# Performance work log

Hardware: AMD Instinct MI355X
Metric: run time of the kernel (lower is better)

Reference implementation:

```python
import jax, jax.numpy as jnp
import numpy as np

B, S, D = 2, 2048, 1024
H = 8
HD = D // H  # 128
RANK = 4
CONTROL_SCALE = 1.0


def setup_inputs() -> dict:
    key = jax.random.key(0)
    ks = jax.random.split(key, 8)
    sd = 0.02
    return {
        "hidden_states": jax.random.normal(ks[0], (B, S, D), jnp.float32),
        "control_states": jax.random.normal(ks[1], (B, S, D), jnp.float32),
        "Wq": jax.random.normal(ks[2], (D, D), jnp.float32) * sd,
        "Wk": jax.random.normal(ks[3], (D, D), jnp.float32) * sd,
        "Wv": jax.random.normal(ks[4], (D, D), jnp.float32) * sd,
        "Wo": jax.random.normal(ks[5], (D, D), jnp.float32) * sd,
        "bo": jnp.zeros((D,), jnp.float32),
        "lora_down": jax.random.normal(ks[6], (RANK, D), jnp.float32) * sd,
        "lora_up": jax.random.normal(ks[7], (D, RANK), jnp.float32) * sd,
    }


def _split_heads(x):  # [B,S,D] -> [B,H,S,HD]
    return x.reshape(B, S, H, HD).transpose(0, 2, 1, 3)


def reference(hidden_states, control_states, Wq, Wk, Wv, Wo, bo, lora_down, lora_up):
    # q/k/v projections (Linear, no bias); self-attention (encoder_hidden_states=None)
    q = _split_heads(jnp.einsum("bsd,ed->bse", hidden_states, Wq))
    k = _split_heads(jnp.einsum("bsd,ed->bse", hidden_states, Wk))
    v = _split_heads(jnp.einsum("bsd,ed->bse", hidden_states, Wv))
    inv_sqrt_d = 1.0 / jnp.sqrt(jnp.asarray(HD, q.dtype))
    scores = jnp.einsum("bhqd,bhkd->bhqk", q, k) * inv_sqrt_d  # [B,H,S,S]
    probs = jax.nn.softmax(scores, axis=-1)
    attn_out = jnp.einsum("bhqk,bhkd->bhqd", probs, v)  # [B,H,S,HD]
    attn_out = attn_out.transpose(0, 2, 1, 3).reshape(B, S, D)
    # to_out[0] Linear with bias; to_out[1] Dropout is identity at eval
    out = jnp.einsum("bsd,ed->bse", attn_out, Wo) + bo
    # LoRA control injection: up(down(control_states))
    ctrl = jnp.einsum("bsr,er->bse", jnp.einsum("bsd,rd->bsr", control_states, lora_down), lora_up)
    return out + CONTROL_SCALE * ctrl
```

## Files before the change

kernel.cpp:

```cpp
#include <hip/hip_runtime.h>
#include <hip/hip_bf16.h>


typedef __bf16 bf8_t __attribute__((ext_vector_type(8)));
typedef float f32x4 __attribute__((ext_vector_type(4)));
typedef float f32x16 __attribute__((ext_vector_type(16)));
typedef unsigned u32x4 __attribute__((ext_vector_type(4)));

#define MFMA16(a, b, c) __builtin_amdgcn_mfma_f32_16x16x32_bf16((a), (b), (c), 0, 0, 0)
#define MFMA32(a, b, c) __builtin_amdgcn_mfma_f32_32x32x16_bf16((a), (b), (c), 0, 0, 0)

__device__ __forceinline__ void gload_lds16(const void* g, void* l) {
  __builtin_amdgcn_global_load_lds(
      (const __attribute__((address_space(1))) void*)g,
      (__attribute__((address_space(3))) void*)l, 16, 0, 0);
}

__device__ __forceinline__ unsigned pk2(float a, float b) {
  unsigned short ua = __builtin_bit_cast(unsigned short, (__bf16)a);
  unsigned short ub = __builtin_bit_cast(unsigned short, (__bf16)b);
  return (unsigned)ua | ((unsigned)ub << 16);
}

__global__ __launch_bounds__(256) void cvt5_k(
    const float* __restrict__ s0, const float* __restrict__ s1,
    const float* __restrict__ s2, const float* __restrict__ s3,
    const float* __restrict__ s4, __bf16* __restrict__ d0,
    __bf16* __restrict__ d1, __bf16* __restrict__ d2, __bf16* __restrict__ d3,
    __bf16* __restrict__ d4) {
  const int which = blockIdx.y;
  const float* s = (which == 0) ? s0 : (which == 1) ? s1 : (which == 2) ? s2
                   : (which == 3) ? s3 : s4;
  __bf16* d = (which == 0) ? d0 : (which == 1) ? d1 : (which == 2) ? d2
              : (which == 3) ? d3 : d4;
  const int n = (which == 0) ? (4096 * 1024) : (1024 * 1024);
  const int i = (blockIdx.x * 256 + threadIdx.x) * 8;
  if (i >= n) return;
  float4 a = *(const float4*)(s + i);
  float4 b = *(const float4*)(s + i + 4);
  bf8_t r;
  r[0] = (__bf16)a.x; r[1] = (__bf16)a.y; r[2] = (__bf16)a.z; r[3] = (__bf16)a.w;
  r[4] = (__bf16)b.x; r[5] = (__bf16)b.y; r[6] = (__bf16)b.z; r[7] = (__bf16)b.w;
  *(bf8_t*)(d + i) = r;
}

__device__ __forceinline__ void gemm_tile(const __bf16* __restrict__ Abase,
                                          const __bf16* __restrict__ Wbase,
                                          int K, __bf16* sA, __bf16* sB,
                                          f32x4 acc[4][4]) {
  const int tid = threadIdx.x;
  const int wave = tid >> 6, lane = tid & 63;
  const int wr = (wave >> 1) * 64, wc = (wave & 1) * 64;
  const int lrow = lane >> 3, lchunk = lane & 7;

  for (int m = 0; m < 4; ++m)
    for (int n = 0; n < 4; ++n)
      acc[m][n] = f32x4{0.f, 0.f, 0.f, 0.f};

  for (int k0 = 0; k0 < K; k0 += 64) {
    for (int i = 0; i < 4; ++i) {
      const int rbase = i * 32 + wave * 8;
      gload_lds16(Abase + (size_t)(rbase + lrow) * K + k0 + lchunk * 8,
                  sA + rbase * 64);
      gload_lds16(Wbase + (size_t)(rbase + lrow) * K + k0 + lchunk * 8,
                  sB + rbase * 64);
    }
    __syncthreads();

    for (int kk = 0; kk < 2; ++kk) {
      bf8_t af[4], bfr[4];
      const int koff = kk * 32 + (lane >> 4) * 8;
      for (int m = 0; m < 4; ++m)
        af[m] = *(const bf8_t*)&sA[(wr + m * 16 + (lane & 15)) * 64 + koff];
      for (int n = 0; n < 4; ++n)
        bfr[n] = *(const bf8_t*)&sB[(wc + n * 16 + (lane & 15)) * 64 + koff];
      for (int m = 0; m < 4; ++m)
        for (int n = 0; n < 4; ++n)
          acc[m][n] = MFMA16(af[m], bfr[n], acc[m][n]);
    }
    __syncthreads();
  }
}

__global__ __launch_bounds__(256) void gemm_qkv_k(
    const __bf16* __restrict__ X, const __bf16* __restrict__ Wq,
    const __bf16* __restrict__ Wk, const __bf16* __restrict__ Wv,
    __bf16* __restrict__ Qb, __bf16* __restrict__ Kb, __bf16* __restrict__ Vtb) {
  __shared__ __bf16 sA[128 * 64];
  __shared__ __bf16 sB[128 * 64];
  const int z = blockIdx.z;
  const int K = 1024;
  int rowT, colT, Nout;
  const __bf16 *Abase, *Wbase;
  __bf16* C;
  if (z == 2) {
    rowT = blockIdx.x; colT = blockIdx.y; Nout = 4096;
    Abase = Wv + (size_t)rowT * 128 * K;
    Wbase = X + (size_t)colT * 128 * K;
    C = Vtb;
  } else {
    rowT = blockIdx.y; colT = blockIdx.x; Nout = 1024;
    Abase = X + (size_t)rowT * 128 * K;
    Wbase = ((z == 0) ? Wq : Wk) + (size_t)colT * 128 * K;
    C = (z == 0) ? Qb : Kb;
  }
  f32x4 acc[4][4];
  gemm_tile(Abase, Wbase, K, sA, sB, acc);

  const int lane = threadIdx.x & 63, wave = threadIdx.x >> 6;
  const int wr = (wave >> 1) * 64, wc = (wave & 1) * 64;
  const int row0 = rowT * 128 + wr + (lane >> 4) * 4;
  const int col0 = colT * 128 + wc + (lane & 15);
  for (int m = 0; m < 4; ++m)
    for (int n = 0; n < 4; ++n)
      for (int j = 0; j < 4; ++j)
        C[(size_t)(row0 + m * 16 + j) * Nout + col0 + n * 16] = (__bf16)acc[m][n][j];
}

__global__ __launch_bounds__(256) void lora_down_k(
    const float* __restrict__ ctrl, const float* __restrict__ down,
    float* __restrict__ tmp) {
  const int tid = threadIdx.x, wave = tid >> 6, lane = tid & 63;
  const int s = blockIdx.x * 4 + wave;
  const float* cp = ctrl + (size_t)s * 1024 + lane * 16;
  float4 c[4];
  for (int i = 0; i < 4; ++i) c[i] = *(const float4*)(cp + i * 4);
  for (int r = 0; r < 4; ++r) {
    const float* dp = down + r * 1024 + lane * 16;
    float acc = 0.f;
    for (int i = 0; i < 4; ++i) {
      float4 dv = *(const float4*)(dp + i * 4);
      acc += c[i].x * dv.x + c[i].y * dv.y + c[i].z * dv.z + c[i].w * dv.w;
    }
    for (int off = 32; off > 0; off >>= 1) acc += __shfl_xor(acc, off);
    if (lane == 0) tmp[s * 4 + r] = acc;
  }
}

__global__ __launch_bounds__(128) void flash_attn_k(
    const __bf16* __restrict__ Qg, const __bf16* __restrict__ Kg,
    const __bf16* __restrict__ Vtg, __bf16* __restrict__ Og) {
  const int S = 2048, D = 1024;
  __shared__ __bf16 sK[2][64 * 128];
  __shared__ __bf16 sVt[2][128 * 64];
  __shared__ float sW[2][32];
  const int qt = blockIdx.x, bh = blockIdx.y;
  const int b = bh >> 3, h = bh & 7;
  const int tid = threadIdx.x, wave = tid >> 6, lane = tid & 63;
  const int l31 = lane & 31, hi = lane >> 5;
  const size_t base = (size_t)b * S * D + (size_t)h * 128;
  const size_t vtbase = (size_t)h * 128 * 4096 + (size_t)b * 2048;
  const int q0 = qt * 64 + wave * 32;

  bf8_t qf[8];
  {
    const float c = 0.08838834764831845f * 1.4426950408889634f;
    const __bf16* qp = Qg + base + (size_t)(q0 + l31) * D + hi * 8;
#pragma unroll
    for (int dc = 0; dc < 8; ++dc) {
      bf8_t v = *(const bf8_t*)(qp + dc * 16);
#pragma unroll
      for (int j = 0; j < 8; ++j) v[j] = (__bf16)((float)v[j] * c);
      qf[dc] = v;
    }
  }

  f32x16 accO[4];
#pragma unroll
  for (int db = 0; db < 4; ++db)
#pragma unroll
    for (int j = 0; j < 16; ++j) accO[db][j] = 0.f;
  float m_ = -1e30f, l_ = 0.f;

  auto stageK = [&](int buf, int kv) {
#pragma unroll
    for (int i = 0; i < 8; ++i) {
      const int r = wave * 32 + i * 4 + (lane >> 4);
      const int gc = (lane & 15) ^ (r & 7);
      gload_lds16(Kg + base + (size_t)(kv + r) * D + gc * 8,
                  &sK[buf][(wave * 32 + i * 4) * 128]);
    }
  };
  auto stageV = [&](int buf, int kv) {
#pragma unroll
    for (int i = 0; i < 8; ++i) {
      const int d = wave * 64 + i * 8 + (lane >> 3);
      const int gc = (lane & 7) ^ (d & 7);
      gload_lds16(Vtg + vtbase + (size_t)d * 4096 + kv + gc * 8,
                  &sVt[buf][(wave * 64 + i * 8) * 64]);
    }
  };

  stageK(0, 0);
  stageV(0, 0);

  for (int t = 0; t < 32; ++t) {
    const int cur = t & 1;
    __syncthreads();
    if (t < 31) {
      stageK(cur ^ 1, (t + 1) * 64);
      stageV(cur ^ 1, (t + 1) * 64);
    }

    f32x16 accS[2];
#pragma unroll
    for (int kb = 0; kb < 2; ++kb)
#pragma unroll
      for (int j = 0; j < 16; ++j) accS[kb][j] = 0.f;
    const __bf16* kb_ = sK[cur];
#pragma unroll
    for (int kb = 0; kb < 2; ++kb) {
      const int kr = kb * 32 + l31;
#pragma unroll
      for (int dc = 0; dc < 8; ++dc) {
        bf8_t a = *(const bf8_t*)&kb_[kr * 128 + ((2 * dc + hi) ^ (kr & 7)) * 8];
        accS[kb] = MFMA32(a, qf[dc], accS[kb]);
      }
    }

    float pm = accS[0][0];
#pragma unroll
    for (int j = 1; j < 16; ++j) pm = fmaxf(pm, accS[0][j]);
#pragma unroll
    for (int j = 0; j < 16; ++j) pm = fmaxf(pm, accS[1][j]);
    pm = fmaxf(pm, __shfl_xor(pm, 32));

    if (__ballot(pm > m_ + 8.0f)) {
      const float mn = fmaxf(m_, pm);
      const float sc = exp2f(m_ - mn);
      m_ = mn;
      l_ *= sc;
      if (hi == 0) sW[wave][l31] = sc;
#pragma unroll
      for (int r = 0; r < 16; ++r) {
        const float scr = sW[wave][(r & 3) + 8 * (r >> 2) + 4 * hi];
#pragma unroll
        for (int db = 0; db < 4; ++db) accO[db][r] *= scr;
      }
    }

    float rs = 0.f;
#pragma unroll
    for (int kb = 0; kb < 2; ++kb)
#pragma unroll
      for (int j = 0; j < 16; ++j) {
        const float p = exp2f(accS[kb][j] - m_);
        accS[kb][j] = p;
        rs += p;
      }
    rs += __shfl_xor(rs, 32);
    l_ += rs;

    unsigned pk[2][4][2];
#pragma unroll
    for (int kb = 0; kb < 2; ++kb)
#pragma unroll
      for (int tq = 0; tq < 4; ++tq) {
        pk[kb][tq][0] = pk2(accS[kb][4 * tq + 0], accS[kb][4 * tq + 1]);
        pk[kb][tq][1] = pk2(accS[kb][4 * tq + 2], accS[kb][4 * tq + 3]);
      }

    const __bf16* vt_ = sVt[cur];
#pragma unroll
    for (int kc = 0; kc < 4; ++kc) {
      const int kb = kc >> 1, par = kc & 1;
      const unsigned own0 = hi ? pk[kb][2 * par + 1][0] : pk[kb][2 * par][0];
      const unsigned own1 = hi ? pk[kb][2 * par + 1][1] : pk[kb][2 * par][1];
      const unsigned snd0 = hi ? pk[kb][2 * par][0] : pk[kb][2 * par + 1][0];
      const unsigned snd1 = hi ? pk[kb][2 * par][1] : pk[kb][2 * par + 1][1];
      const unsigned rc0 = (unsigned)__shfl_xor((int)snd0, 32);
      const unsigned rc1 = (unsigned)__shfl_xor((int)snd1, 32);
      u32x4 fr;
      fr[0] = hi ? rc0 : own0;
      fr[1] = hi ? rc1 : own1;
      fr[2] = hi ? own0 : rc0;
      fr[3] = hi ? own1 : rc1;
      const bf8_t pa = __builtin_bit_cast(bf8_t, fr);
#pragma unroll
      for (int db = 0; db < 4; ++db) {
        const int dr = db * 32 + l31;
        bf8_t vb = *(const bf8_t*)&vt_[dr * 64 + ((2 * kc + hi) ^ (dr & 7)) * 8];
        accO[db] = MFMA32(pa, vb, accO[db]);
      }
    }
  }

  if (hi == 0) sW[wave][l31] = l_;
#pragma unroll
  for (int r = 0; r < 16; ++r) {
    const int qr = (r & 3) + 8 * (r >> 2) + 4 * hi;
    const float linv = 1.0f / sW[wave][qr];
    __bf16* op = Og + base + (size_t)(q0 + qr) * D + l31;
#pragma unroll
    for (int db = 0; db < 4; ++db)
      op[db * 32] = (__bf16)(accO[db][r] * linv);
  }
}

__global__ __launch_bounds__(256) void gemm_out_k(
    const __bf16* __restrict__ A, const __bf16* __restrict__ Wo,
    const float* __restrict__ bo, const float* __restrict__ lup,
    const float* __restrict__ tmp, float* __restrict__ out) {
  __shared__ __bf16 sA[128 * 64];
  __shared__ __bf16 sB[128 * 64];
  const int bcol = blockIdx.x, brow = blockIdx.y;
  const int K = 1024, N = 1024;
  f32x4 acc[4][4];
  gemm_tile(A + (size_t)brow * 128 * K, Wo + (size_t)bcol * 128 * K, K, sA, sB, acc);

  const int lane = threadIdx.x & 63, wave = threadIdx.x >> 6;
  const int wr = (wave >> 1) * 64, wc = (wave & 1) * 64;
  for (int n = 0; n < 4; ++n) {
    const int col = bcol * 128 + wc + n * 16 + (lane & 15);
    const float bias = bo[col];
    const float u0 = lup[col * 4 + 0], u1 = lup[col * 4 + 1];
    const float u2 = lup[col * 4 + 2], u3 = lup[col * 4 + 3];
    for (int m = 0; m < 4; ++m)
      for (int j = 0; j < 4; ++j) {
        const int row = brow * 128 + wr + m * 16 + (lane >> 4) * 4 + j;
        const float* t = tmp + row * 4;
        float v = acc[m][n][j] + bias + t[0] * u0 + t[1] * u1 + t[2] * u2 + t[3] * u3;
        out[(size_t)row * N + col] = v;
      }
  }
}

extern "C" void kernel_launch(void* const* d_in, const int* in_sizes, int n_in,
                              void* d_out, int out_size, void* d_ws, size_t ws_size,
                              hipStream_t stream) {
  (void)in_sizes; (void)n_in; (void)out_size; (void)ws_size;
  const float* hs  = (const float*)d_in[0];
  const float* cs  = (const float*)d_in[1];
  const float* Wq  = (const float*)d_in[2];
  const float* Wk  = (const float*)d_in[3];
  const float* Wv  = (const float*)d_in[4];
  const float* Wo  = (const float*)d_in[5];
  const float* bo  = (const float*)d_in[6];
  const float* ldw = (const float*)d_in[7];
  const float* lup = (const float*)d_in[8];
  float* out = (float*)d_out;

  const size_t MD = (size_t)4096 * 1024;
  const size_t WD = (size_t)1024 * 1024;
  __bf16* hsb = (__bf16*)d_ws;
  __bf16* Wqb = hsb + MD;
  __bf16* Wkb = Wqb + WD;
  __bf16* Wvb = Wkb + WD;
  __bf16* Wob = Wvb + WD;
  __bf16* Qb  = Wob + WD;
  __bf16* Kb  = Qb + MD;
  __bf16* Vtb = Kb + MD;
  __bf16* Ab  = Vtb + MD;
  float*  tmp = (float*)(Ab + MD);

  cvt5_k<<<dim3(2048, 5), 256, 0, stream>>>(hs, Wq, Wk, Wv, Wo,
                                            hsb, Wqb, Wkb, Wvb, Wob);
  gemm_qkv_k<<<dim3(8, 32, 3), 256, 0, stream>>>(hsb, Wqb, Wkb, Wvb, Qb, Kb, Vtb);
  lora_down_k<<<dim3(1024), 256, 0, stream>>>(cs, ldw, tmp);
  flash_attn_k<<<dim3(32, 16), 128, 0, stream>>>(Qb, Kb, Vtb, Ab);
  gemm_out_k<<<dim3(8, 32), 256, 0, stream>>>(Ab, Wob, bo, lup, tmp, out);
}
```

Before: 176.0 us.

## Split attention KV range across two blocks and merge partial results

```diff
diff --git a/kernel.cpp b/kernel.cpp
--- a/kernel.cpp
+++ b/kernel.cpp
@@ -139,18 +139,20 @@
 
 __global__ __launch_bounds__(128) void flash_attn_k(
     const __bf16* __restrict__ Qg, const __bf16* __restrict__ Kg,
-    const __bf16* __restrict__ Vtg, __bf16* __restrict__ Og) {
+    const __bf16* __restrict__ Vtg, __bf16* __restrict__ Op,
+    float* __restrict__ ml) {
   const int S = 2048, D = 1024;
-  __shared__ __bf16 sK[2][64 * 128];
-  __shared__ __bf16 sVt[2][128 * 64];
+  __shared__ __bf16 sK[2][32 * 128];
+  __shared__ __bf16 sVt[2][128 * 32];
   __shared__ float sW[2][32];
-  const int qt = blockIdx.x, bh = blockIdx.y;
+  const int qt = blockIdx.x, bh = blockIdx.y, z = blockIdx.z;
   const int b = bh >> 3, h = bh & 7;
   const int tid = threadIdx.x, wave = tid >> 6, lane = tid & 63;
   const int l31 = lane & 31, hi = lane >> 5;
   const size_t base = (size_t)b * S * D + (size_t)h * 128;
   const size_t vtbase = (size_t)h * 128 * 4096 + (size_t)b * 2048;
   const int q0 = qt * 64 + wave * 32;
+  const int kvbase = z * 1024;
 
   bf8_t qf[8];
   {
@@ -174,55 +176,48 @@
 
   auto stageK = [&](int buf, int kv) {
 #pragma unroll
-    for (int i = 0; i < 8; ++i) {
-      const int r = wave * 32 + i * 4 + (lane >> 4);
+    for (int i = 0; i < 4; ++i) {
+      const int r = wave * 16 + i * 4 + (lane >> 4);
       const int gc = (lane & 15) ^ (r & 7);
       gload_lds16(Kg + base + (size_t)(kv + r) * D + gc * 8,
-                  &sK[buf][(wave * 32 + i * 4) * 128]);
+                  &sK[buf][(wave * 16 + i * 4) * 128]);
     }
   };
   auto stageV = [&](int buf, int kv) {
 #pragma unroll
-    for (int i = 0; i < 8; ++i) {
-      const int d = wave * 64 + i * 8 + (lane >> 3);
-      const int gc = (lane & 7) ^ (d & 7);
+    for (int i = 0; i < 4; ++i) {
+      const int d = wave * 64 + i * 16 + (lane >> 2);
+      const int gc = (lane & 3) ^ (d & 3);
       gload_lds16(Vtg + vtbase + (size_t)d * 4096 + kv + gc * 8,
-                  &sVt[buf][(wave * 64 + i * 8) * 64]);
+                  &sVt[buf][(wave * 64 + i * 16) * 32]);
     }
   };
 
-  stageK(0, 0);
-  stageV(0, 0);
+  stageK(0, kvbase);
+  stageV(0, kvbase);
 
   for (int t = 0; t < 32; ++t) {
     const int cur = t & 1;
     __syncthreads();
     if (t < 31) {
-      stageK(cur ^ 1, (t + 1) * 64);
-      stageV(cur ^ 1, (t + 1) * 64);
-    }
-
-    f32x16 accS[2];
-#pragma unroll
-    for (int kb = 0; kb < 2; ++kb)
-#pragma unroll
-      for (int j = 0; j < 16; ++j) accS[kb][j] = 0.f;
+      stageK(cur ^ 1, kvbase + (t + 1) * 32);
+      stageV(cur ^ 1, kvbase + (t + 1) * 32);
+    }
+
+    f32x16 accS;
+#pragma unroll
+    for (int j = 0; j < 16; ++j) accS[j] = 0.f;
     const __bf16* kb_ = sK[cur];
-#pragma unroll
-    for (int kb = 0; kb < 2; ++kb) {
-      const int kr = kb * 32 + l31;
-#pragma unroll
-      for (int dc = 0; dc < 8; ++dc) {
-        bf8_t a = *(const bf8_t*)&kb_[kr * 128 + ((2 * dc + hi) ^ (kr & 7)) * 8];
-        accS[kb] = MFMA32(a, qf[dc], accS[kb]);
-      }
-    }
-
-    float pm = accS[0][0];
-#pragma unroll
-    for (int j = 1; j < 16; ++j) pm = fmaxf(pm, accS[0][j]);
-#pragma unroll
-    for (int j = 0; j < 16; ++j) pm = fmaxf(pm, accS[1][j]);
+    const int kr = l31;
+#pragma unroll
+    for (int dc = 0; dc < 8; ++dc) {
+      bf8_t a = *(const bf8_t*)&kb_[kr * 128 + ((2 * dc + hi) ^ (kr & 7)) * 8];
+      accS = MFMA32(a, qf[dc], accS);
+    }
+
+    float pm = accS[0];
+#pragma unroll
+    for (int j = 1; j < 16; ++j) pm = fmaxf(pm, accS[j]);
     pm = fmaxf(pm, __shfl_xor(pm, 32));
 
     if (__ballot(pm > m_ + 8.0f)) {
@@ -241,33 +236,28 @@
 
     float rs = 0.f;
 #pragma unroll
-    for (int kb = 0; kb < 2; ++kb)
-#pragma unroll
-      for (int j = 0; j < 16; ++j) {
-        const float p = exp2f(accS[kb][j] - m_);
-        accS[kb][j] = p;
-        rs += p;
-      }
+    for (int j = 0; j < 16; ++j) {
+      const float p = exp2f(accS[j] - m_);
+      accS[j] = p;
+      rs += p;
+    }
     rs += __shfl_xor(rs, 32);
     l_ += rs;
 
-    unsigned pk[2][4][2];
-#pragma unroll
-    for (int kb = 0; kb < 2; ++kb)
-#pragma unroll
-      for (int tq = 0; tq < 4; ++tq) {
-        pk[kb][tq][0] = pk2(accS[kb][4 * tq + 0], accS[kb][4 * tq + 1]);
-        pk[kb][tq][1] = pk2(accS[kb][4 * tq + 2], accS[kb][4 * tq + 3]);
-      }
+    unsigned pk[4][2];
+#pragma unroll
+    for (int tq = 0; tq < 4; ++tq) {
+      pk[tq][0] = pk2(accS[4 * tq + 0], accS[4 * tq + 1]);
+      pk[tq][1] = pk2(accS[4 * tq + 2], accS[4 * tq + 3]);
+    }
 
     const __bf16* vt_ = sVt[cur];
 #pragma unroll
-    for (int kc = 0; kc < 4; ++kc) {
-      const int kb = kc >> 1, par = kc & 1;
-      const unsigned own0 = hi ? pk[kb][2 * par + 1][0] : pk[kb][2 * par][0];
-      const unsigned own1 = hi ? pk[kb][2 * par + 1][1] : pk[kb][2 * par][1];
-      const unsigned snd0 = hi ? pk[kb][2 * par][0] : pk[kb][2 * par + 1][0];
-      const unsigned snd1 = hi ? pk[kb][2 * par][1] : pk[kb][2 * par + 1][1];
+    for (int kc = 0; kc < 2; ++kc) {
+      const unsigned own0 = hi ? pk[2 * kc + 1][0] : pk[2 * kc][0];
+      const unsigned own1 = hi ? pk[2 * kc + 1][1] : pk[2 * kc][1];
+      const unsigned snd0 = hi ? pk[2 * kc][0] : pk[2 * kc + 1][0];
+      const unsigned snd1 = hi ? pk[2 * kc][1] : pk[2 * kc + 1][1];
       const unsigned rc0 = (unsigned)__shfl_xor((int)snd0, 32);
       const unsigned rc1 = (unsigned)__shfl_xor((int)snd1, 32);
       u32x4 fr;
@@ -279,22 +269,51 @@
 #pragma unroll
       for (int db = 0; db < 4; ++db) {
         const int dr = db * 32 + l31;
-        bf8_t vb = *(const bf8_t*)&vt_[dr * 64 + ((2 * kc + hi) ^ (dr & 7)) * 8];
+        bf8_t vb = *(const bf8_t*)&vt_[dr * 32 + ((kc * 2 + hi) ^ (dr & 3)) * 8];
         accO[db] = MFMA32(pa, vb, accO[db]);
       }
     }
   }
 
-  if (hi == 0) sW[wave][l31] = l_;
+  const size_t pbase = ((size_t)(z * 16 + bh) * 2048 + q0);
 #pragma unroll
   for (int r = 0; r < 16; ++r) {
     const int qr = (r & 3) + 8 * (r >> 2) + 4 * hi;
-    const float linv = 1.0f / sW[wave][qr];
-    __bf16* op = Og + base + (size_t)(q0 + qr) * D + l31;
+    __bf16* op = Op + (pbase + qr) * 128 + l31;
 #pragma unroll
     for (int db = 0; db < 4; ++db)
-      op[db * 32] = (__bf16)(accO[db][r] * linv);
-  }
+      op[db * 32] = (__bf16)(accO[db][r]);
+  }
+  if (hi == 0) {
+    ml[(pbase + l31) * 2 + 0] = m_;
+    ml[(pbase + l31) * 2 + 1] = l_;
+  }
+}
+
+__global__ __launch_bounds__(256) void attn_merge_k(
+    const __bf16* __restrict__ Op, const float* __restrict__ ml,
+    __bf16* __restrict__ Og) {
+  const int bh = blockIdx.x >> 7, qc = blockIdx.x & 127;
+  const int t = threadIdx.x;
+  const int qr = qc * 16 + (t >> 4);
+  const int d0 = (t & 15) * 8;
+  const int b = bh >> 3, h = bh & 7;
+
+  const size_t i0 = ((size_t)bh * 2048 + qr);
+  const size_t i1 = ((size_t)(16 + bh) * 2048 + qr);
+  const float m0 = ml[i0 * 2], l0 = ml[i0 * 2 + 1];
+  const float m1 = ml[i1 * 2], l1 = ml[i1 * 2 + 1];
+  const float m = fmaxf(m0, m1);
+  const float w0 = exp2f(m0 - m), w1 = exp2f(m1 - m);
+  const float inv = 1.0f / (l0 * w0 + l1 * w1);
+
+  bf8_t o0 = *(const bf8_t*)(Op + i0 * 128 + d0);
+  bf8_t o1 = *(const bf8_t*)(Op + i1 * 128 + d0);
+  bf8_t r;
+#pragma unroll
+  for (int j = 0; j < 8; ++j)
+    r[j] = (__bf16)(((float)o0[j] * w0 + (float)o1[j] * w1) * inv);
+  *(bf8_t*)(Og + ((size_t)(b * 2048 + qr) * 1024) + h * 128 + d0) = r;
 }
 
 __global__ __launch_bounds__(256) void gemm_out_k(
@@ -352,11 +371,14 @@
   __bf16* Vtb = Kb + MD;
   __bf16* Ab  = Vtb + MD;
   float*  tmp = (float*)(Ab + MD);
+  __bf16* Opart = (__bf16*)(tmp + 4096 * 4);
+  float*  mlp   = (float*)(Opart + (size_t)2 * 16 * 2048 * 128);
 
   cvt5_k<<<dim3(2048, 5), 256, 0, stream>>>(hs, Wq, Wk, Wv, Wo,
                                             hsb, Wqb, Wkb, Wvb, Wob);
   gemm_qkv_k<<<dim3(8, 32, 3), 256, 0, stream>>>(hsb, Wqb, Wkb, Wvb, Qb, Kb, Vtb);
   lora_down_k<<<dim3(1024), 256, 0, stream>>>(cs, ldw, tmp);
-  flash_attn_k<<<dim3(32, 16), 128, 0, stream>>>(Qb, Kb, Vtb, Ab);
+  flash_attn_k<<<dim3(32, 16, 2), 128, 0, stream>>>(Qb, Kb, Vtb, Opart, mlp);
+  attn_merge_k<<<dim3(2048), 256, 0, stream>>>(Opart, mlp, Ab);
   gemm_out_k<<<dim3(8, 32), 256, 0, stream>>>(Ab, Wob, bo, lup, tmp, out);
 }
```

New measurement: 169.2 us. 1.04x faster.
